# Optimization experiments

Hardware: AMD Instinct MI355X
Metric: run time of the kernel (lower is better)

Reference implementation:

```python
import jax, jax.numpy as jnp
import numpy as np

DIM = 1024
FACTOR = 32          # factor_size
SUB = 8              # sub_blocks = (dim // factor_size) // 4
RANK = 8
B, T = 48, 256


def hamilton(A_stack):
    # A_stack: (rank, 4, SUB, SUB) -> H: (rank, 4*SUB, 4*SUB)
    r, i, j, k = A_stack[:, 0], A_stack[:, 1], A_stack[:, 2], A_stack[:, 3]
    row0 = jnp.concatenate([r, -i, -j, -k], axis=2)
    row1 = jnp.concatenate([i,  r, -k,  j], axis=2)
    row2 = jnp.concatenate([j,  k,  r, -i], axis=2)
    row3 = jnp.concatenate([k, -j,  i,  r], axis=2)
    return jnp.concatenate([row0, row1, row2, row3], axis=1)


def setup_inputs() -> dict:
    key = jax.random.key(0)
    k1, k2, k3 = jax.random.split(key, 3)
    x = jax.random.normal(k1, (B, T, DIM), dtype=jnp.float32)
    A_stack = jax.random.normal(k2, (RANK, 4, SUB, SUB), dtype=jnp.float32)
    # factors_B: orthogonal-init then scaled by (rank_index)^-0.5; random normal
    # scaled similarly is numerically equivalent in structure for the reference.
    scales = (jnp.arange(1, RANK + 1, dtype=jnp.float32) ** -0.5)[:, None, None]
    B_stack = jax.random.normal(k3, (RANK, FACTOR, FACTOR), dtype=jnp.float32) * scales
    bias = jnp.zeros((DIM,), dtype=jnp.float32)
    return {"x": x, "A_stack": A_stack, "B_stack": B_stack, "bias": bias}


def reference(x, A_stack, B_stack, bias):
    Bb, Tt, D = x.shape
    x_flat = x.reshape(-1, 4 * SUB, FACTOR)           # (n, 32, 32)
    H = hamilton(A_stack)                              # (r, 32, 32)
    wave_mod = jnp.einsum('nsi,rji->rnsj', x_flat, B_stack)   # (r, n, 32, 32)
    wave_out = jnp.einsum('rnsj,rks->nkj', wave_mod, H)       # (n, 32, 32)
    return wave_out.reshape(Bb, Tt, D) + bias
```

## Files before the change

kernel.cpp:

```cpp
#include <hip/hip_runtime.h>
#include <hip/hip_bf16.h>
#include <stdint.h>

#define M_TOT 12288
#define K_DIM 1024
#define N_DIM 1024

typedef __attribute__((ext_vector_type(8))) __bf16 bf16x8;
typedef __attribute__((ext_vector_type(4))) float  f32x4;

__global__ __launch_bounds__(256)
void make_w(const float* __restrict__ A4,
            const float* __restrict__ Bs,
            __bf16* __restrict__ W)
{
    int idx = blockIdx.x * 256 + threadIdx.x;
    int dout = idx >> 10;
    int din  = idx & 1023;
    int k = dout >> 5, j = dout & 31;
    int s = din  >> 5, i = din  & 31;
    int kb = k >> 3, k8 = k & 7;
    int sb = s >> 3, s8 = s & 7;

    const int   comp[4][4] = {{0,1,2,3},{1,0,3,2},{2,3,0,1},{3,2,1,0}};
    const float sgn [4][4] = {{1.f,-1.f,-1.f,-1.f},
                              {1.f, 1.f,-1.f, 1.f},
                              {1.f, 1.f, 1.f,-1.f},
                              {1.f,-1.f, 1.f, 1.f}};
    int   c  = comp[kb][sb];
    float sg = sgn [kb][sb];

    float acc = 0.f;
    #pragma unroll
    for (int r = 0; r < 8; ++r) {
        float h = A4[((r*4 + c)*8 + k8)*8 + s8];
        float b = Bs[(r*32 + j)*32 + i];
        acc += h * b;
    }
    W[idx] = (__bf16)(sg * acc);
}

__global__ __launch_bounds__(256)
void cvt_x(const float* __restrict__ X, __bf16* __restrict__ Xb)
{
    size_t t = (size_t)blockIdx.x * 256 + threadIdx.x;
    const float4* x4 = (const float4*)X;
    float4 a = x4[2*t + 0];
    float4 b = x4[2*t + 1];
    bf16x8 v;
    v[0] = (__bf16)a.x; v[1] = (__bf16)a.y; v[2] = (__bf16)a.z; v[3] = (__bf16)a.w;
    v[4] = (__bf16)b.x; v[5] = (__bf16)b.y; v[6] = (__bf16)b.z; v[7] = (__bf16)b.w;
    *(bf16x8*)&Xb[t * 8] = v;
}

#define BM 128
#define BN 128
#define BK 32

__device__ __forceinline__ void gl_lds16(const void* g, void* l)
{
    __builtin_amdgcn_global_load_lds(
        (const __attribute__((address_space(1))) void*)g,
        (__attribute__((address_space(3))) void*)l,
        16, 0, 0);
}

__global__ __launch_bounds__(256)
void gemm_bt(const __bf16* __restrict__ A,
             const __bf16* __restrict__ BT,
             const float*  __restrict__ bias,
             float* __restrict__ C)
{
    __shared__ __align__(16) __bf16 Alds[BM * BK];
    __shared__ __align__(16) __bf16 Blds[BN * BK];

    const int tid  = threadIdx.x;
    const int wave = tid >> 6;
    const int lane = tid & 63;

    const int brow = blockIdx.y * BM;
    const int bcol = blockIdx.x * BN;

    const int wm = (wave >> 1) * 64;
    const int wn = (wave & 1)  * 64;

    f32x4 acc[4][4];
    #pragma unroll
    for (int i = 0; i < 4; ++i)
        #pragma unroll
        for (int jj = 0; jj < 4; ++jj)
            acc[i][jj] = (f32x4){0.f, 0.f, 0.f, 0.f};

    const int fr = lane & 15;
    const int kq = lane >> 4;

    char* AldsC = (char*)Alds;
    char* BldsC = (char*)Blds;

    for (int k0 = 0; k0 < K_DIM; k0 += BK) {
        #pragma unroll
        for (int q = 0; q < 2; ++q) {
            int ofs  = wave * 2048 + q * 1024 + lane * 16;
            int row  = ofs >> 6;
            int colb = ofs & 63;
            gl_lds16((const char*)A  + ((size_t)(brow + row) * K_DIM + k0) * 2 + colb,
                     AldsC + wave * 2048 + q * 1024);
            gl_lds16((const char*)BT + ((size_t)(bcol + row) * K_DIM + k0) * 2 + colb,
                     BldsC + wave * 2048 + q * 1024);
        }
        __syncthreads();

        bf16x8 af[4], bfr[4];
        #pragma unroll
        for (int mi = 0; mi < 4; ++mi)
            af[mi] = *(const bf16x8*)&Alds[(wm + mi*16 + fr) * BK + kq * 8];
        #pragma unroll
        for (int ni = 0; ni < 4; ++ni)
            bfr[ni] = *(const bf16x8*)&Blds[(wn + ni*16 + fr) * BK + kq * 8];

        #pragma unroll
        for (int mi = 0; mi < 4; ++mi)
            #pragma unroll
            for (int ni = 0; ni < 4; ++ni)
                acc[mi][ni] = __builtin_amdgcn_mfma_f32_16x16x32_bf16(
                    af[mi], bfr[ni], acc[mi][ni], 0, 0, 0);

        __syncthreads();
    }

    #pragma unroll
    for (int mi = 0; mi < 4; ++mi) {
        int r0 = brow + wm + mi*16 + (lane >> 4) * 4;
        #pragma unroll
        for (int ni = 0; ni < 4; ++ni) {
            int c0 = bcol + wn + ni*16 + (lane & 15);
            float bv = bias[c0];
            #pragma unroll
            for (int j = 0; j < 4; ++j)
                C[(size_t)(r0 + j) * N_DIM + c0] = acc[mi][ni][j] + bv;
        }
    }
}

extern "C" void kernel_launch(void* const* d_in, const int* in_sizes, int n_in,
                              void* d_out, int out_size, void* d_ws, size_t ws_size,
                              hipStream_t stream)
{
    const float* x    = (const float*)d_in[0];
    const float* A4   = (const float*)d_in[1];
    const float* Bs   = (const float*)d_in[2];
    const float* bias = (const float*)d_in[3];
    float* out = (float*)d_out;

    __bf16* W  = (__bf16*)d_ws;
    __bf16* Xb = (__bf16*)((char*)d_ws + (size_t)(1<<21));

    make_w<<<4096, 256, 0, stream>>>(A4, Bs, W);
    cvt_x<<<(M_TOT * K_DIM / 8 + 255) / 256, 256, 0, stream>>>(x, Xb);

    dim3 grid(N_DIM / BN, M_TOT / BM);
    gemm_bt<<<grid, 256, 0, stream>>>(Xb, W, bias, out);
}
```

Before: 136.9 us.

## Replace GEMM with 256x256 8-wave ping-pong pipelined kernel using swizzled LDS

Replaces the simple 128x128 single-buffered GEMM with a 256x256 tile, 512-thread kernel that double-buffers 64-wide K tiles in 128KB of LDS. Global-to-LDS loads for the next tiles are interleaved with four MFMA phases, using explicit barriers, waitcnt and setprio. LDS uses XOR swizzling to avoid bank conflicts, and the workgroup index is remapped for L2 locality. The aim is to hide memory latency and raise MFMA utilisation. In exchange it adds heavy register pressure and fragile hand-written synchronisation.

```diff
diff --git a/kernel.cpp b/kernel.cpp
--- a/kernel.cpp
+++ b/kernel.cpp
@@ -5,6 +5,7 @@
 #define M_TOT 12288
 #define K_DIM 1024
 #define N_DIM 1024
+#define NTILE 16
 
 typedef __attribute__((ext_vector_type(8))) __bf16 bf16x8;
 typedef __attribute__((ext_vector_type(4))) float  f32x4;
@@ -53,10 +54,6 @@
     *(bf16x8*)&Xb[t * 8] = v;
 }
 
-#define BM 128
-#define BN 128
-#define BK 32
-
 __device__ __forceinline__ void gl_lds16(const void* g, void* l)
 {
     __builtin_amdgcn_global_load_lds(
@@ -65,79 +62,162 @@
         16, 0, 0);
 }
 
-__global__ __launch_bounds__(256)
-void gemm_bt(const __bf16* __restrict__ A,
-             const __bf16* __restrict__ BT,
-             const float*  __restrict__ bias,
-             float* __restrict__ C)
-{
-    __shared__ __align__(16) __bf16 Alds[BM * BK];
-    __shared__ __align__(16) __bf16 Blds[BN * BK];
+#define PHASE_MFMA(MH, NH, BF)                                                  \
+    __builtin_amdgcn_s_barrier();                                               \
+    asm volatile("s_waitcnt lgkmcnt(0)" ::: "memory");                          \
+    __builtin_amdgcn_sched_barrier(0);                                          \
+    __builtin_amdgcn_s_setprio(1);                                              \
+    _Pragma("unroll")                                                           \
+    for (int mi = 0; mi < 4; ++mi) {                                            \
+        _Pragma("unroll")                                                       \
+        for (int ni = 0; ni < 2; ++ni) {                                        \
+            acc[(MH)*4+mi][(NH)*2+ni] = __builtin_amdgcn_mfma_f32_16x16x32_bf16(\
+                aF[mi][0], BF[ni][0], acc[(MH)*4+mi][(NH)*2+ni], 0, 0, 0);      \
+            acc[(MH)*4+mi][(NH)*2+ni] = __builtin_amdgcn_mfma_f32_16x16x32_bf16(\
+                aF[mi][1], BF[ni][1], acc[(MH)*4+mi][(NH)*2+ni], 0, 0, 0);      \
+        }                                                                       \
+    }                                                                           \
+    __builtin_amdgcn_s_setprio(0);                                              \
+    __builtin_amdgcn_s_barrier();
+
+__global__ __launch_bounds__(512, 2)
+void gemm8p(const __bf16* __restrict__ A,
+            const __bf16* __restrict__ BT,
+            const float*  __restrict__ bias,
+            float* __restrict__ C)
+{
+    __shared__ __align__(16) char lds[131072];
 
     const int tid  = threadIdx.x;
     const int wave = tid >> 6;
     const int lane = tid & 63;
 
-    const int brow = blockIdx.y * BM;
-    const int bcol = blockIdx.x * BN;
-
-    const int wm = (wave >> 1) * 64;
-    const int wn = (wave & 1)  * 64;
-
-    f32x4 acc[4][4];
-    #pragma unroll
-    for (int i = 0; i < 4; ++i)
-        #pragma unroll
-        for (int jj = 0; jj < 4; ++jj)
-            acc[i][jj] = (f32x4){0.f, 0.f, 0.f, 0.f};
-
+    int wg  = blockIdx.x;
+    int swz = (wg & 7) * 24 + (wg >> 3);
+    const int brow = (swz >> 2) * 256;
+    const int bcol = (swz & 3)  * 256;
+
+    const int mg = wave >> 2;
+    const int ng = wave & 3;
     const int fr = lane & 15;
     const int kq = lane >> 4;
 
-    char* AldsC = (char*)Alds;
-    char* BldsC = (char*)Blds;
-
-    for (int k0 = 0; k0 < K_DIM; k0 += BK) {
+    f32x4 acc[8][4];
+    #pragma unroll
+    for (int i = 0; i < 8; ++i)
+        #pragma unroll
+        for (int j = 0; j < 4; ++j)
+            acc[i][j] = (f32x4){0.f, 0.f, 0.f, 0.f};
+
+    auto stageA = [&](int ta, int mh) {
+        if (ta >= NTILE) return;
+        char* region = lds + (ta & 1) * 65536 + mh * 16384;
         #pragma unroll
         for (int q = 0; q < 2; ++q) {
-            int ofs  = wave * 2048 + q * 1024 + lane * 16;
-            int row  = ofs >> 6;
-            int colb = ofs & 63;
-            gl_lds16((const char*)A  + ((size_t)(brow + row) * K_DIM + k0) * 2 + colb,
-                     AldsC + wave * 2048 + q * 1024);
-            gl_lds16((const char*)BT + ((size_t)(bcol + row) * K_DIM + k0) * 2 + colb,
-                     BldsC + wave * 2048 + q * 1024);
-        }
-        __syncthreads();
-
-        bf16x8 af[4], bfr[4];
-        #pragma unroll
-        for (int mi = 0; mi < 4; ++mi)
-            af[mi] = *(const bf16x8*)&Alds[(wm + mi*16 + fr) * BK + kq * 8];
-        #pragma unroll
-        for (int ni = 0; ni < 4; ++ni)
-            bfr[ni] = *(const bf16x8*)&Blds[(wn + ni*16 + fr) * BK + kq * 8];
-
-        #pragma unroll
-        for (int mi = 0; mi < 4; ++mi)
-            #pragma unroll
-            for (int ni = 0; ni < 4; ++ni)
-                acc[mi][ni] = __builtin_amdgcn_mfma_f32_16x16x32_bf16(
-                    af[mi], bfr[ni], acc[mi][ni], 0, 0, 0);
-
-        __syncthreads();
+            int s    = q * 8192 + tid * 16;
+            int rwh  = s >> 7;
+            int colb = (s & 127) ^ ((rwh & 7) << 4);
+            int absr = ((rwh >> 6) << 7) + mh * 64 + (rwh & 63);
+            const char* src = (const char*)A +
+                ((size_t)(brow + absr) * K_DIM + ta * 64) * 2 + colb;
+            gl_lds16(src, region + q * 8192 + wave * 1024);
+        }
+    };
+    auto stageB = [&](int ta, int nh) {
+        if (ta >= NTILE) return;
+        char* region = lds + (ta & 1) * 65536 + 32768 + nh * 16384;
+        #pragma unroll
+        for (int q = 0; q < 2; ++q) {
+            int s    = q * 8192 + tid * 16;
+            int rwh  = s >> 7;
+            int colb = (s & 127) ^ ((rwh & 7) << 4);
+            int absr = ((rwh >> 5) << 6) + nh * 32 + (rwh & 31);
+            const char* src = (const char*)BT +
+                ((size_t)(bcol + absr) * K_DIM + ta * 64) * 2 + colb;
+            gl_lds16(src, region + q * 8192 + wave * 1024);
+        }
+    };
+
+    bf16x8 aF[4][2], bF0[2][2], bF1[2][2];
+
+    auto ldA = [&](int bufb, int mh) {
+        const char* base = lds + bufb + mh * 16384;
+        #pragma unroll
+        for (int mi = 0; mi < 4; ++mi) {
+            int rwh = mg * 64 + mi * 16 + fr;
+            #pragma unroll
+            for (int ks = 0; ks < 2; ++ks) {
+                int col = (ks * 64 + kq * 16) ^ ((rwh & 7) << 4);
+                aF[mi][ks] = *(const bf16x8*)(base + rwh * 128 + col);
+            }
+        }
+    };
+    auto ldB = [&](bf16x8 (&bF)[2][2], int bufb, int nh) {
+        const char* base = lds + bufb + 32768 + nh * 16384;
+        #pragma unroll
+        for (int ni = 0; ni < 2; ++ni) {
+            int rwh = ng * 32 + ni * 16 + fr;
+            #pragma unroll
+            for (int ks = 0; ks < 2; ++ks) {
+                int col = (ks * 64 + kq * 16) ^ ((rwh & 7) << 4);
+                bF[ni][ks] = *(const bf16x8*)(base + rwh * 128 + col);
+            }
+        }
+    };
+
+    stageA(0, 0); stageA(0, 1); stageB(0, 0); stageB(0, 1);
+    stageA(1, 0); stageA(1, 1);
+    asm volatile("s_waitcnt vmcnt(4)" ::: "memory");
+    __builtin_amdgcn_s_barrier();
+
+    for (int t = 0; t < NTILE; ++t) {
+        const int bufb = (t & 1) * 65536;
+
+        ldA(bufb, 0);
+        ldB(bF0, bufb, 0);
+        stageB(t + 1, 0);
+        PHASE_MFMA(0, 0, bF0)
+
+        ldB(bF1, bufb, 1);
+        stageB(t + 1, 1);
+        PHASE_MFMA(0, 1, bF1)
+
+        ldA(bufb, 1);
+        stageA(t + 2, 0);
+        PHASE_MFMA(1, 1, bF1)
+
+        stageA(t + 2, 1);
+        __builtin_amdgcn_s_barrier();
+        __builtin_amdgcn_s_setprio(1);
+        #pragma unroll
+        for (int mi = 0; mi < 4; ++mi) {
+            #pragma unroll
+            for (int ni = 0; ni < 2; ++ni) {
+                acc[4+mi][ni] = __builtin_amdgcn_mfma_f32_16x16x32_bf16(
+                    aF[mi][0], bF0[ni][0], acc[4+mi][ni], 0, 0, 0);
+                acc[4+mi][ni] = __builtin_amdgcn_mfma_f32_16x16x32_bf16(
+                    aF[mi][1], bF0[ni][1], acc[4+mi][ni], 0, 0, 0);
+            }
+        }
+        __builtin_amdgcn_s_setprio(0);
+        if (t < NTILE - 2) {
+            asm volatile("s_waitcnt vmcnt(4)" ::: "memory");
+        } else {
+            asm volatile("s_waitcnt vmcnt(0)" ::: "memory");
+        }
+        __builtin_amdgcn_s_barrier();
     }
 
     #pragma unroll
-    for (int mi = 0; mi < 4; ++mi) {
-        int r0 = brow + wm + mi*16 + (lane >> 4) * 4;
-        #pragma unroll
-        for (int ni = 0; ni < 4; ++ni) {
-            int c0 = bcol + wn + ni*16 + (lane & 15);
+    for (int mf = 0; mf < 8; ++mf) {
+        int r0 = brow + mg * 128 + mf * 16 + kq * 4;
+        #pragma unroll
+        for (int nf = 0; nf < 4; ++nf) {
+            int c0 = bcol + ng * 64 + nf * 16 + fr;
             float bv = bias[c0];
             #pragma unroll
             for (int j = 0; j < 4; ++j)
-                C[(size_t)(r0 + j) * N_DIM + c0] = acc[mi][ni][j] + bv;
+                C[(size_t)(r0 + j) * N_DIM + c0] = acc[mf][nf][j] + bv;
         }
     }
 }
@@ -158,6 +238,5 @@
     make_w<<<4096, 256, 0, stream>>>(A4, Bs, W);
     cvt_x<<<(M_TOT * K_DIM / 8 + 255) / 256, 256, 0, stream>>>(x, Xb);
 
-    dim3 grid(N_DIM / BN, M_TOT / BM);
-    gemm_bt<<<grid, 256, 0, stream>>>(Xb, W, bias, out);
-}
+    gemm8p<<<192, 512, 0, stream>>>(Xb, W, bias, out);
+}
```

New measurement: 133.5 us. 2.5% less time.
